# Performance work log

Hardware: AMD Instinct MI355X
Metric: run time of the kernel (lower is better)

## Reference

```python
import jax, jax.numpy as jnp
import numpy as np

DIM_IN = 1024
DIM_OUT = 1024


def setup_inputs() -> dict:
    key = jax.random.key(0)
    k_x, k_q, k_k, k_v = jax.random.split(key, 4)
    B, S = 4, 2048
    scale = 1.0 / np.sqrt(DIM_IN)
    X = jax.random.normal(k_x, (B, S, DIM_IN), dtype=jnp.float32)
    # nn.Linear weights stored as [out, in]; forward is X @ W.T
    W_q = jax.random.normal(k_q, (DIM_OUT, DIM_IN), dtype=jnp.float32) * scale
    W_k = jax.random.normal(k_k, (DIM_OUT, DIM_IN), dtype=jnp.float32) * scale
    W_v = jax.random.normal(k_v, (DIM_OUT, DIM_IN), dtype=jnp.float32) * scale
    return {"X": X, "W_q": W_q, "W_k": W_k, "W_v": W_v}


def reference(X, W_q, W_k, W_v):
    # Q, K, V: [B, S, D]
    Q = jnp.einsum('bsd,ed->bse', X, W_q)
    K = jnp.einsum('bsd,ed->bse', X, W_k)
    V = jnp.einsum('bsd,ed->bse', X, W_v)
    S = X.shape[1]
    scores = jnp.einsum('bqe,bke->bqk', Q, K)  # [B, S, S]
    # causal mask: strictly upper triangle -> -inf (applied before scaling, as in source)
    causal = jnp.triu(jnp.ones((S, S), dtype=bool), k=1)
    scores = jnp.where(causal[None, :, :], -jnp.inf, scores)
    scores = scores / jnp.sqrt(jnp.asarray(K.shape[-1], dtype=scores.dtype))
    weights = jax.nn.softmax(scores, axis=-1)
    # dropout_p = 0.0 (eval mode) -> identity
    return jnp.einsum('bqk,bke->bqe', weights, V)
```

## Files before the change

### kernel.cpp

```cpp
#include <hip/hip_runtime.h>
#include <hip/hip_bf16.h>
#include <hip/hip_fp16.h>
#include <stdint.h>

#define NBATCH 4
#define SEQ    2048
#define DIM    1024

typedef __attribute__((ext_vector_type(8))) __bf16 bf16x8;
typedef __attribute__((ext_vector_type(4))) float  f32x4;

#define OFF_XBF   (0ull)
#define OFF_WBF   (16777216ull)
#define OFF_Q     (23068672ull)
#define OFF_K     (39845888ull)
#define OFF_VT    (56623104ull)
#define OFF_SC    (73400320ull)
#define OFF_P     (140509184ull)

__device__ __forceinline__ uint16_t f2bf(float f) {
  uint32_t u = __float_as_uint(f);
  u = (u + 0x7fffu + ((u >> 16) & 1u)) >> 16;
  return (uint16_t)u;
}

__global__ __launch_bounds__(256) void k_convert(const float* __restrict__ X,
                                                 const float* __restrict__ Wq,
                                                 const float* __restrict__ Wk,
                                                 const float* __restrict__ Wv,
                                                 uint16_t* __restrict__ Xbf,
                                                 uint16_t* __restrict__ Wbf) {
  int id = blockIdx.x;
  if (id < 8192) {
    int i = id * 256 + threadIdx.x;
    float4 v = ((const float4*)X)[i];
    ushort4 o;
    o.x = f2bf(v.x); o.y = f2bf(v.y); o.z = f2bf(v.z); o.w = f2bf(v.w);
    ((ushort4*)Xbf)[i] = o;
  } else {
    int j = id - 8192;
    int g = j >> 10;
    const float* W = (g == 0) ? Wq : (g == 1) ? Wk : Wv;
    float scale = (g == 0) ? 0.03125f : 1.0f;
    int i = (j & 1023) * 256 + threadIdx.x;
    float4 v = ((const float4*)W)[i];
    ushort4 o;
    o.x = f2bf(v.x * scale); o.y = f2bf(v.y * scale);
    o.z = f2bf(v.z * scale); o.w = f2bf(v.w * scale);
    ((ushort4*)(Wbf + (size_t)g * 1048576))[i] = o;
  }
}


__device__ __forceinline__ void gll16(const void* g, void* l) {
  __builtin_amdgcn_global_load_lds((const __attribute__((address_space(1))) void*)g,
                                   (__attribute__((address_space(3))) void*)l, 16, 0, 0);
}

__device__ __forceinline__ bf16x8 frag_ld(const char* lds, int row, int kbyte) {
  int bo = row * 128 + kbyte;
  bo ^= (row & 7) << 4;
  return *(const bf16x8*)(lds + bo);
}

#define VM_WAIT8() asm volatile("s_waitcnt vmcnt(8)" ::: "memory")
#define VM_WAIT0() asm volatile("s_waitcnt vmcnt(0)" ::: "memory")
#define RAW_BAR()  asm volatile("s_barrier" ::: "memory")

__device__ __forceinline__ void stage_tile(const uint16_t* __restrict__ g, int ld,
                                           int t, char* lds) {
#pragma unroll
  for (int c = 0; c < 4; ++c) {
    int L = c * 4096 + t * 16;
    int row = L >> 7;
    int slot = (t & 7) ^ (row & 7);
    gll16((const void*)(g + (size_t)row * ld + slot * 8), (void*)(lds + L));
  }
}

__device__ __forceinline__ void gemm_loop(const uint16_t* __restrict__ A, int lda,
                                          const uint16_t* __restrict__ Bm, int ldb,
                                          int ksteps, char* lds, f32x4 acc[4][4]) {
  char* lA0 = lds;          char* lA1 = lds + 16384;
  char* lB0 = lds + 32768;  char* lB1 = lds + 49152;
  const int t = threadIdx.x;
  const int lane = t & 63;
  const int wm = (t >> 6) & 1;
  const int wn = t >> 7;
  const int frow = lane & 15;
  const int fk16 = (lane >> 4) * 16;

  stage_tile(A,      lda, t, lA0); stage_tile(Bm,      ldb, t, lB0);
  if (ksteps > 1) { stage_tile(A + 64, lda, t, lA1); stage_tile(Bm + 64, ldb, t, lB1); }

  for (int kt = 0; kt < ksteps; ++kt) {
    if (kt == ksteps - 1) { VM_WAIT0(); } else { VM_WAIT8(); }
    RAW_BAR();
    const char* cA = (kt & 1) ? lA1 : lA0;
    const char* cB = (kt & 1) ? lB1 : lB0;
#pragma unroll
    for (int ki = 0; ki < 2; ++ki) {
      bf16x8 av[4], bv[4];
#pragma unroll
      for (int mi = 0; mi < 4; ++mi)
        av[mi] = frag_ld(cA, wm * 64 + mi * 16 + frow, ki * 64 + fk16);
#pragma unroll
      for (int ni = 0; ni < 4; ++ni)
        bv[ni] = frag_ld(cB, wn * 64 + ni * 16 + frow, ki * 64 + fk16);
      __builtin_amdgcn_s_setprio(1);
#pragma unroll
      for (int mi = 0; mi < 4; ++mi)
#pragma unroll
        for (int ni = 0; ni < 4; ++ni)
          acc[mi][ni] = __builtin_amdgcn_mfma_f32_16x16x32_bf16(av[mi], bv[ni],
                                                                acc[mi][ni], 0, 0, 0);
      __builtin_amdgcn_s_setprio(0);
    }
    RAW_BAR();
    if (kt + 2 < ksteps) {
      stage_tile(A  + (kt + 2) * 64, lda, t, (kt & 1) ? lA1 : lA0);
      stage_tile(Bm + (kt + 2) * 64, ldb, t, (kt & 1) ? lB1 : lB0);
    }
  }
}

__global__ __launch_bounds__(256) void k_qkv(const uint16_t* __restrict__ Xbf,
                                             const uint16_t* __restrict__ Wbf,
                                             uint16_t* __restrict__ Qb,
                                             uint16_t* __restrict__ Kb,
                                             uint16_t* __restrict__ Vt) {
  __shared__ __align__(16) char lds[65536];
  int id = blockIdx.x;
  const int mt = id & 63, nt = id >> 6;
  const int m0 = mt * 128, n0 = nt * 128;
  const int g = n0 >> 10, ncol = n0 & 1023;

  f32x4 acc[4][4];
#pragma unroll
  for (int i = 0; i < 4; ++i)
#pragma unroll
    for (int j = 0; j < 4; ++j) acc[i][j] = (f32x4){0.f, 0.f, 0.f, 0.f};

  const uint16_t* A  = Xbf + (size_t)m0 * DIM;
  const uint16_t* Bm = Wbf + (size_t)n0 * DIM;
  gemm_loop(A, DIM, Bm, DIM, DIM / 64, lds, acc);

  const int lane = threadIdx.x & 63;
  const int wm = (threadIdx.x >> 6) & 1, wn = threadIdx.x >> 7;
  const int rbase = wm * 64 + (lane >> 4) * 4;
  const int cbase = wn * 64 + (lane & 15);

  if (g < 2) {
    uint16_t* out = (g == 0) ? Qb : Kb;
#pragma unroll
    for (int mi = 0; mi < 4; ++mi)
#pragma unroll
      for (int ni = 0; ni < 4; ++ni) {
        int c = ncol + cbase + ni * 16;
#pragma unroll
        for (int r = 0; r < 4; ++r) {
          int m = m0 + rbase + mi * 16 + r;
          out[(size_t)m * DIM + c] = f2bf(acc[mi][ni][r]);
        }
      }
  } else {
    const int b = m0 >> 11, sl = m0 & 2047;
#pragma unroll
    for (int mi = 0; mi < 4; ++mi)
#pragma unroll
      for (int ni = 0; ni < 4; ++ni) {
        int e = ncol + cbase + ni * 16;
        int s = sl + rbase + mi * 16;
        ushort4 o;
        o.x = f2bf(acc[mi][ni][0]); o.y = f2bf(acc[mi][ni][1]);
        o.z = f2bf(acc[mi][ni][2]); o.w = f2bf(acc[mi][ni][3]);
        *(ushort4*)(Vt + ((size_t)b * DIM + e) * SEQ + s) = o;
      }
  }
}

__global__ __launch_bounds__(256) void k_scores(const uint16_t* __restrict__ Qb,
                                                const uint16_t* __restrict__ Kb,
                                                __half* __restrict__ Sc) {
  __shared__ __align__(16) char lds[65536];
  int x = blockIdx.x;
  int b = x / 136, tr = x % 136;
  int qt = 0;
  while ((qt + 1) * (qt + 2) / 2 <= tr) ++qt;
  int kt = tr - qt * (qt + 1) / 2;

  f32x4 acc[4][4];
#pragma unroll
  for (int i = 0; i < 4; ++i)
#pragma unroll
    for (int j = 0; j < 4; ++j) acc[i][j] = (f32x4){0.f, 0.f, 0.f, 0.f};

  const uint16_t* A = Qb + ((size_t)b * SEQ + qt * 128) * DIM;
  const uint16_t* Bm = Kb + ((size_t)b * SEQ + kt * 128) * DIM;
  gemm_loop(A, DIM, Bm, DIM, DIM / 64, lds, acc);

  const int lane = threadIdx.x & 63;
  const int wm = (threadIdx.x >> 6) & 1, wn = threadIdx.x >> 7;
  const int rbase = qt * 128 + wm * 64 + (lane >> 4) * 4;
  const int cbase = kt * 128 + wn * 64 + (lane & 15);
  __half* out = Sc + (size_t)b * SEQ * SEQ;
#pragma unroll
  for (int mi = 0; mi < 4; ++mi)
#pragma unroll
    for (int ni = 0; ni < 4; ++ni) {
      int c = cbase + ni * 16;
#pragma unroll
      for (int r = 0; r < 4; ++r)
        out[(size_t)(rbase + mi * 16 + r) * SEQ + c] = __float2half(acc[mi][ni][r]);
    }
}

struct h4 { __half2 a, b; };

__global__ __launch_bounds__(256) void k_softmax(const __half* __restrict__ Sc,
                                                 uint16_t* __restrict__ P) {
  int gid = blockIdx.x * 4 + (threadIdx.x >> 6);
  int lane = threadIdx.x & 63;
  int b = gid >> 11, q = gid & 2047;
  const __half* srow = Sc + ((size_t)b * SEQ + q) * SEQ;
  uint16_t* prow = P + ((size_t)b * SEQ + q) * SEQ;
  int nv = q + 1;
  int kpad = ((q >> 7) + 1) << 7;
  int niter = (kpad + 255) >> 8;

  float4 v[8];
  const h4* src = (const h4*)srow;
#pragma unroll
  for (int i = 0; i < 8; ++i) {
    if (i < niter) {
      int idx = lane + (i << 6);
      h4 raw = src[idx];
      float2 fa = __half22float2(raw.a), fb = __half22float2(raw.b);
      int k0 = idx << 2;
      float4 x;
      x.x = (k0 + 0 < nv) ? fa.x : -1e38f;
      x.y = (k0 + 1 < nv) ? fa.y : -1e38f;
      x.z = (k0 + 2 < nv) ? fb.x : -1e38f;
      x.w = (k0 + 3 < nv) ? fb.y : -1e38f;
      v[i] = x;
    } else {
      v[i] = make_float4(-1e38f, -1e38f, -1e38f, -1e38f);
    }
  }
  float m = -1e38f;
#pragma unroll
  for (int i = 0; i < 8; ++i)
    m = fmaxf(m, fmaxf(fmaxf(v[i].x, v[i].y), fmaxf(v[i].z, v[i].w)));
#pragma unroll
  for (int o = 32; o > 0; o >>= 1) m = fmaxf(m, __shfl_xor(m, o));

  float s = 0.f;
#pragma unroll
  for (int i = 0; i < 8; ++i) {
    v[i].x = __expf(v[i].x - m); v[i].y = __expf(v[i].y - m);
    v[i].z = __expf(v[i].z - m); v[i].w = __expf(v[i].w - m);
    s += v[i].x + v[i].y + v[i].z + v[i].w;
  }
#pragma unroll
  for (int o = 32; o > 0; o >>= 1) s += __shfl_xor(s, o);
  float inv = 1.0f / s;

  ushort4* dst = (ushort4*)prow;
#pragma unroll
  for (int i = 0; i < 8; ++i) {
    if (i < niter) {
      int idx = lane + (i << 6);
      if ((idx << 2) < kpad) {
        ushort4 o;
        o.x = f2bf(v[i].x * inv); o.y = f2bf(v[i].y * inv);
        o.z = f2bf(v[i].z * inv); o.w = f2bf(v[i].w * inv);
        dst[idx] = o;
      }
    }
  }
}

__global__ __launch_bounds__(256) void k_pv(const uint16_t* __restrict__ P,
                                            const uint16_t* __restrict__ Vt,
                                            float* __restrict__ O) {
  __shared__ __align__(16) char lds[65536];
  int x = blockIdx.x;
  int b = x >> 7, r7 = x & 127;
  int qt = 15 - (r7 >> 3);
  int et = r7 & 7;

  f32x4 acc[4][4];
#pragma unroll
  for (int i = 0; i < 4; ++i)
#pragma unroll
    for (int j = 0; j < 4; ++j) acc[i][j] = (f32x4){0.f, 0.f, 0.f, 0.f};

  const uint16_t* A = P + (size_t)b * SEQ * SEQ + (size_t)qt * 128 * SEQ;
  const uint16_t* Bm = Vt + (size_t)b * DIM * SEQ + (size_t)et * 128 * SEQ;
  gemm_loop(A, SEQ, Bm, SEQ, (qt + 1) * 2, lds, acc);

  const int lane = threadIdx.x & 63;
  const int wm = (threadIdx.x >> 6) & 1, wn = threadIdx.x >> 7;
  const int rbase = qt * 128 + wm * 64 + (lane >> 4) * 4;
  const int cbase = et * 128 + wn * 64 + (lane & 15);
  float* out = O + (size_t)b * SEQ * DIM;
#pragma unroll
  for (int mi = 0; mi < 4; ++mi)
#pragma unroll
    for (int ni = 0; ni < 4; ++ni) {
      int c = cbase + ni * 16;
#pragma unroll
      for (int r = 0; r < 4; ++r)
        out[(size_t)(rbase + mi * 16 + r) * DIM + c] = acc[mi][ni][r];
    }
}

extern "C" void kernel_launch(void* const* d_in, const int* in_sizes, int n_in,
                              void* d_out, int out_size, void* d_ws, size_t ws_size,
                              hipStream_t stream) {
  const float* X  = (const float*)d_in[0];
  const float* Wq = (const float*)d_in[1];
  const float* Wk = (const float*)d_in[2];
  const float* Wv = (const float*)d_in[3];
  char* ws = (char*)d_ws;
  uint16_t* Xbf = (uint16_t*)(ws + OFF_XBF);
  uint16_t* Wbf = (uint16_t*)(ws + OFF_WBF);
  uint16_t* Qb  = (uint16_t*)(ws + OFF_Q);
  uint16_t* Kb  = (uint16_t*)(ws + OFF_K);
  uint16_t* Vt  = (uint16_t*)(ws + OFF_VT);
  __half*   Sc  = (__half*)(ws + OFF_SC);
  uint16_t* P   = (uint16_t*)(ws + OFF_P);
  float*    O   = (float*)d_out;

  k_convert<<<11264, 256, 0, stream>>>(X, Wq, Wk, Wv, Xbf, Wbf);
  k_qkv<<<1536, 256, 0, stream>>>(Xbf, Wbf, Qb, Kb, Vt);
  k_scores<<<544, 256, 0, stream>>>(Qb, Kb, Sc);
  k_softmax<<<2048, 256, 0, stream>>>(Sc, P);
  k_pv<<<512, 256, 0, stream>>>(P, Vt, O);
}
```

Measured before the change: 160.5 us.

## Restructure QKV GEMM into 128x256 tiles with 8 waves and interleaved loads

The QKV projection kernel now uses 512-thread blocks with 128x256 output tiles, a 128-wide K step and 96KB of dynamic LDS. The loads for the next K step are split into partial sweeps and issued between two half-phases of MFMA work, each half covering two of the four N subtiles. The goal is more reuse of each A tile and better overlap of global-to-LDS copies with matrix math. In exchange there are more barriers per step and more LDS per block, which may limit occupancy. The hand-tuned vmcnt waits add correctness risk.

```diff
diff --git a/kernel.cpp b/kernel.cpp
--- a/kernel.cpp
+++ b/kernel.cpp
@@ -64,8 +64,162 @@
 }
 
 #define VM_WAIT8() asm volatile("s_waitcnt vmcnt(8)" ::: "memory")
+#define VM_WAIT3() asm volatile("s_waitcnt vmcnt(3)" ::: "memory")
 #define VM_WAIT0() asm volatile("s_waitcnt vmcnt(0)" ::: "memory")
 #define RAW_BAR()  asm volatile("s_barrier" ::: "memory")
+
+
+__device__ __forceinline__ void sweepA(const uint16_t* __restrict__ Ab, int kt,
+                                       int t, char* ldsA) {
+#pragma unroll
+  for (int c = 0; c < 2; ++c) {
+    int L = c * 8192 + t * 16;
+    int row = L >> 7;
+    int slot = (t & 7) ^ (row & 7);
+    gll16((const void*)(Ab + (size_t)row * DIM + kt * 64 + slot * 8),
+          (void*)(ldsA + L));
+  }
+}
+__device__ __forceinline__ void sweepB(const uint16_t* __restrict__ Bb, int kt,
+                                       int t, char* ldsB, int sb, int off) {
+  int strip = sb + (t >> 8);
+  int rl = (t >> 3) & 31;
+  int grow = strip * 64 + off + rl;
+  int slot = (t & 7) ^ (grow & 7);
+  gll16((const void*)(Bb + (size_t)grow * DIM + kt * 64 + slot * 8),
+        (void*)(ldsB + grow * 128 + (t & 7) * 16));
+}
+
+__global__ __launch_bounds__(512, 2) void k_qkv(const uint16_t* __restrict__ Xbf,
+                                                const uint16_t* __restrict__ Wbf,
+                                                uint16_t* __restrict__ Qb,
+                                                uint16_t* __restrict__ Kb,
+                                                uint16_t* __restrict__ Vt) {
+  extern __shared__ char lds[];
+  char* A0 = lds;           char* B0 = lds + 16384;
+  char* A1 = lds + 49152;   char* B1 = lds + 65536;
+
+  const int t = threadIdx.x;
+  const int lane = t & 63;
+  const int wid = t >> 6;
+  const int wm = wid >> 2;
+  const int wn = wid & 3;
+  const int frow = lane & 15;
+  const int fk16 = (lane >> 4) * 16;
+
+  int id = blockIdx.x;
+  const int mt = id & 63, nt = id >> 6;
+  const int m0 = mt * 128, n0 = nt * 256;
+  const int g = n0 >> 10, ncol = n0 & 1023;
+
+  const uint16_t* A  = Xbf + (size_t)m0 * DIM;
+  const uint16_t* Bm = Wbf + (size_t)n0 * DIM;
+
+  f32x4 acc[4][4];
+#pragma unroll
+  for (int i = 0; i < 4; ++i)
+#pragma unroll
+    for (int j = 0; j < 4; ++j) acc[i][j] = (f32x4){0.f, 0.f, 0.f, 0.f};
+
+  sweepA(A, 0, t, A0);
+  sweepB(Bm, 0, t, B0, 0, 0);  sweepB(Bm, 0, t, B0, 2, 0);
+  sweepB(Bm, 0, t, B0, 0, 32); sweepB(Bm, 0, t, B0, 2, 32);
+  sweepA(A, 1, t, A1);
+  sweepB(Bm, 1, t, B1, 0, 0);
+  VM_WAIT3(); RAW_BAR();
+
+#pragma unroll 1
+  for (int kt = 0; kt < 16; ++kt) {
+    char* cA = (kt & 1) ? A1 : A0;
+    char* cB = (kt & 1) ? B1 : B0;
+    char* nB = (kt & 1) ? B0 : B1;
+
+    bf16x8 av[4][2], bv01[2][2];
+#pragma unroll
+    for (int mi = 0; mi < 4; ++mi)
+#pragma unroll
+      for (int ki = 0; ki < 2; ++ki)
+        av[mi][ki] = frag_ld(cA, wm * 64 + mi * 16 + frow, ki * 64 + fk16);
+#pragma unroll
+    for (int ni = 0; ni < 2; ++ni)
+#pragma unroll
+      for (int ki = 0; ki < 2; ++ki)
+        bv01[ni][ki] = frag_ld(cB, wn * 64 + ni * 16 + frow, ki * 64 + fk16);
+    if (kt <= 14) {
+      sweepB(Bm, kt + 1, t, nB, 2, 0);
+      sweepB(Bm, kt + 1, t, nB, 0, 32);
+      sweepB(Bm, kt + 1, t, nB, 2, 32);
+    }
+    RAW_BAR();
+    __builtin_amdgcn_s_setprio(1);
+#pragma unroll
+    for (int mi = 0; mi < 4; ++mi)
+#pragma unroll
+      for (int ni = 0; ni < 2; ++ni)
+#pragma unroll
+        for (int ki = 0; ki < 2; ++ki)
+          acc[mi][ni] = __builtin_amdgcn_mfma_f32_16x16x32_bf16(av[mi][ki], bv01[ni][ki],
+                                                                acc[mi][ni], 0, 0, 0);
+    __builtin_amdgcn_s_setprio(0);
+    RAW_BAR();
+
+    bf16x8 bv23[2][2];
+#pragma unroll
+    for (int ni = 0; ni < 2; ++ni)
+#pragma unroll
+      for (int ki = 0; ki < 2; ++ki)
+        bv23[ni][ki] = frag_ld(cB, wn * 64 + (2 + ni) * 16 + frow, ki * 64 + fk16);
+    if (kt <= 13) {
+      sweepA(A, kt + 2, t, cA);
+      sweepB(Bm, kt + 2, t, cB, 0, 0);
+    }
+    if (kt <= 13)      { VM_WAIT3(); }
+    else if (kt == 14) { VM_WAIT0(); }
+    RAW_BAR();
+    __builtin_amdgcn_s_setprio(1);
+#pragma unroll
+    for (int mi = 0; mi < 4; ++mi)
+#pragma unroll
+      for (int ni = 0; ni < 2; ++ni)
+#pragma unroll
+        for (int ki = 0; ki < 2; ++ki)
+          acc[mi][2 + ni] = __builtin_amdgcn_mfma_f32_16x16x32_bf16(av[mi][ki], bv23[ni][ki],
+                                                                    acc[mi][2 + ni], 0, 0, 0);
+    __builtin_amdgcn_s_setprio(0);
+    RAW_BAR();
+  }
+
+  const int rbase = wm * 64 + (lane >> 4) * 4;
+  const int cbase = wn * 64 + (lane & 15);
+
+  if (g < 2) {
+    uint16_t* out = (g == 0) ? Qb : Kb;
+#pragma unroll
+    for (int mi = 0; mi < 4; ++mi)
+#pragma unroll
+      for (int ni = 0; ni < 4; ++ni) {
+        int c = ncol + cbase + ni * 16;
+#pragma unroll
+        for (int r = 0; r < 4; ++r) {
+          int m = m0 + rbase + mi * 16 + r;
+          out[(size_t)m * DIM + c] = f2bf(acc[mi][ni][r]);
+        }
+      }
+  } else {
+    const int b = m0 >> 11, sl = m0 & 2047;
+#pragma unroll
+    for (int mi = 0; mi < 4; ++mi)
+#pragma unroll
+      for (int ni = 0; ni < 4; ++ni) {
+        int e = ncol + cbase + ni * 16;
+        int s = sl + rbase + mi * 16;
+        ushort4 o;
+        o.x = f2bf(acc[mi][ni][0]); o.y = f2bf(acc[mi][ni][1]);
+        o.z = f2bf(acc[mi][ni][2]); o.w = f2bf(acc[mi][ni][3]);
+        *(ushort4*)(Vt + ((size_t)b * DIM + e) * SEQ + s) = o;
+      }
+  }
+}
 
 __device__ __forceinline__ void stage_tile(const uint16_t* __restrict__ g, int ld,
                                            int t, char* lds) {
@@ -121,61 +275,6 @@
       stage_tile(A  + (kt + 2) * 64, lda, t, (kt & 1) ? lA1 : lA0);
       stage_tile(Bm + (kt + 2) * 64, ldb, t, (kt & 1) ? lB1 : lB0);
     }
-  }
-}
-
-__global__ __launch_bounds__(256) void k_qkv(const uint16_t* __restrict__ Xbf,
-                                             const uint16_t* __restrict__ Wbf,
-                                             uint16_t* __restrict__ Qb,
-                                             uint16_t* __restrict__ Kb,
-                                             uint16_t* __restrict__ Vt) {
-  __shared__ __align__(16) char lds[65536];
-  int id = blockIdx.x;
-  const int mt = id & 63, nt = id >> 6;
-  const int m0 = mt * 128, n0 = nt * 128;
-  const int g = n0 >> 10, ncol = n0 & 1023;
-
-  f32x4 acc[4][4];
-#pragma unroll
-  for (int i = 0; i < 4; ++i)
-#pragma unroll
-    for (int j = 0; j < 4; ++j) acc[i][j] = (f32x4){0.f, 0.f, 0.f, 0.f};
-
-  const uint16_t* A  = Xbf + (size_t)m0 * DIM;
-  const uint16_t* Bm = Wbf + (size_t)n0 * DIM;
-  gemm_loop(A, DIM, Bm, DIM, DIM / 64, lds, acc);
-
-  const int lane = threadIdx.x & 63;
-  const int wm = (threadIdx.x >> 6) & 1, wn = threadIdx.x >> 7;
-  const int rbase = wm * 64 + (lane >> 4) * 4;
-  const int cbase = wn * 64 + (lane & 15);
-
-  if (g < 2) {
-    uint16_t* out = (g == 0) ? Qb : Kb;
-#pragma unroll
-    for (int mi = 0; mi < 4; ++mi)
-#pragma unroll
-      for (int ni = 0; ni < 4; ++ni) {
-        int c = ncol + cbase + ni * 16;
-#pragma unroll
-        for (int r = 0; r < 4; ++r) {
-          int m = m0 + rbase + mi * 16 + r;
-          out[(size_t)m * DIM + c] = f2bf(acc[mi][ni][r]);
-        }
-      }
-  } else {
-    const int b = m0 >> 11, sl = m0 & 2047;
-#pragma unroll
-    for (int mi = 0; mi < 4; ++mi)
-#pragma unroll
-      for (int ni = 0; ni < 4; ++ni) {
-        int e = ncol + cbase + ni * 16;
-        int s = sl + rbase + mi * 16;
-        ushort4 o;
-        o.x = f2bf(acc[mi][ni][0]); o.y = f2bf(acc[mi][ni][1]);
-        o.z = f2bf(acc[mi][ni][2]); o.w = f2bf(acc[mi][ni][3]);
-        *(ushort4*)(Vt + ((size_t)b * DIM + e) * SEQ + s) = o;
-      }
   }
 }
 
@@ -333,7 +432,7 @@
   float*    O   = (float*)d_out;
 
   k_convert<<<11264, 256, 0, stream>>>(X, Wq, Wk, Wv, Xbf, Wbf);
-  k_qkv<<<1536, 256, 0, stream>>>(Xbf, Wbf, Qb, Kb, Vt);
+  k_qkv<<<768, 512, 98304, stream>>>(Xbf, Wbf, Qb, Kb, Vt);
   k_scores<<<544, 256, 0, stream>>>(Qb, Kb, Sc);
   k_softmax<<<2048, 256, 0, stream>>>(Sc, P);
   k_pv<<<512, 256, 0, stream>>>(P, Vt, O);
```

Measured after the change: 165.7 us. +3.3%, slower.

## Use 256x256 tiles with 8 waves and 128KB LDS for QKV GEMM

Applied to the files above, without the earlier changes.

Replaces the 128x128, 256-thread QKV projection GEMM with a 256x256 tile per 512-thread block. It double-buffers 128KB of dynamic LDS and issues the next k-tile's half-tile loads between MFMA quadrants, so each loaded tile feeds more MFMAs and prefetch overlaps compute. It also reorders the k_pv block index so heavy and light causal rows from different batches interleave across the grid. Costs: only one block per CU and 384 blocks, which risks tail imbalance, plus the dynamic LDS size may need an attribute to exceed the default limit.

```diff
diff --git a/kernel.cpp b/kernel.cpp
--- a/kernel.cpp
+++ b/kernel.cpp
@@ -67,6 +67,184 @@
 #define VM_WAIT0() asm volatile("s_waitcnt vmcnt(0)" ::: "memory")
 #define RAW_BAR()  asm volatile("s_barrier" ::: "memory")
 
+
+__device__ __forceinline__ void stage_half(const uint16_t* __restrict__ g,
+                                           int t, char* ldsH) {
+#pragma unroll
+  for (int c = 0; c < 2; ++c) {
+    int L = c * 8192 + t * 16;
+    int row = L >> 7;
+    int slot = (t & 7) ^ (row & 7);
+    gll16((const void*)(g + (size_t)row * DIM + slot * 8), (void*)(ldsH + L));
+  }
+}
+
+template<int CUR>
+__device__ __forceinline__ void qkv_ktile(char* lds, const uint16_t* __restrict__ A,
+                                          const uint16_t* __restrict__ Bm,
+                                          int t, int wm, int wn, int frow, int fk16,
+                                          int kt, f32x4 (&acc)[8][4]) {
+  char* base = lds + CUR * 65536;
+  const char* Ah0 = base;
+  const char* Ah1 = base + 16384;
+  const char* Bh  = base + 32768 + (wn >> 1) * 16384;
+  const int brow = (wn & 1) * 64;
+  const bool stage_on = (kt <= 13);
+  const int k2 = (kt + 2) * 64;
+
+  bf16x8 av[4][2], bv01[2][2], bv23[2][2];
+
+  if (kt == 15) { VM_WAIT0(); } else { VM_WAIT8(); }
+  RAW_BAR();
+#pragma unroll
+  for (int mq = 0; mq < 4; ++mq)
+#pragma unroll
+    for (int ki = 0; ki < 2; ++ki)
+      av[mq][ki] = frag_ld(Ah0, wm * 64 + mq * 16 + frow, ki * 64 + fk16);
+#pragma unroll
+  for (int nq = 0; nq < 2; ++nq)
+#pragma unroll
+    for (int ki = 0; ki < 2; ++ki)
+      bv01[nq][ki] = frag_ld(Bh, brow + nq * 16 + frow, ki * 64 + fk16);
+  __builtin_amdgcn_s_setprio(1);
+#pragma unroll
+  for (int mq = 0; mq < 4; ++mq)
+#pragma unroll
+    for (int nq = 0; nq < 2; ++nq)
+#pragma unroll
+      for (int ki = 0; ki < 2; ++ki)
+        acc[mq][nq] = __builtin_amdgcn_mfma_f32_16x16x32_bf16(av[mq][ki], bv01[nq][ki],
+                                                              acc[mq][nq], 0, 0, 0);
+  __builtin_amdgcn_s_setprio(0);
+  RAW_BAR();
+
+#pragma unroll
+  for (int nq = 0; nq < 2; ++nq)
+#pragma unroll
+    for (int ki = 0; ki < 2; ++ki)
+      bv23[nq][ki] = frag_ld(Bh, brow + 32 + nq * 16 + frow, ki * 64 + fk16);
+  if (stage_on) stage_half(A + k2, t, base + 0);
+  __builtin_amdgcn_s_setprio(1);
+#pragma unroll
+  for (int mq = 0; mq < 4; ++mq)
+#pragma unroll
+    for (int nq = 0; nq < 2; ++nq)
+#pragma unroll
+      for (int ki = 0; ki < 2; ++ki)
+        acc[mq][2 + nq] = __builtin_amdgcn_mfma_f32_16x16x32_bf16(av[mq][ki], bv23[nq][ki],
+                                                                  acc[mq][2 + nq], 0, 0, 0);
+  __builtin_amdgcn_s_setprio(0);
+  RAW_BAR();
+
+#pragma unroll
+  for (int mq = 0; mq < 4; ++mq)
+#pragma unroll
+    for (int ki = 0; ki < 2; ++ki)
+      av[mq][ki] = frag_ld(Ah1, wm * 64 + mq * 16 + frow, ki * 64 + fk16);
+  if (stage_on) {
+    stage_half(Bm + k2,             t, base + 32768);
+    stage_half(Bm + 128 * DIM + k2, t, base + 49152);
+  }
+  __builtin_amdgcn_s_setprio(1);
+#pragma unroll
+  for (int mq = 0; mq < 4; ++mq)
+#pragma unroll
+    for (int nq = 0; nq < 2; ++nq)
+#pragma unroll
+      for (int ki = 0; ki < 2; ++ki)
+        acc[4 + mq][nq] = __builtin_amdgcn_mfma_f32_16x16x32_bf16(av[mq][ki], bv01[nq][ki],
+                                                                  acc[4 + mq][nq], 0, 0, 0);
+  __builtin_amdgcn_s_setprio(0);
+  RAW_BAR();
+
+  if (stage_on) stage_half(A + 128 * DIM + k2, t, base + 16384);
+  __builtin_amdgcn_s_setprio(1);
+#pragma unroll
+  for (int mq = 0; mq < 4; ++mq)
+#pragma unroll
+    for (int nq = 0; nq < 2; ++nq)
+#pragma unroll
+      for (int ki = 0; ki < 2; ++ki)
+        acc[4 + mq][2 + nq] = __builtin_amdgcn_mfma_f32_16x16x32_bf16(av[mq][ki], bv23[nq][ki],
+                                                                      acc[4 + mq][2 + nq], 0, 0, 0);
+  __builtin_amdgcn_s_setprio(0);
+  RAW_BAR();
+}
+
+__global__ __launch_bounds__(512, 1) void k_qkv(const uint16_t* __restrict__ Xbf,
+                                                const uint16_t* __restrict__ Wbf,
+                                                uint16_t* __restrict__ Qb,
+                                                uint16_t* __restrict__ Kb,
+                                                uint16_t* __restrict__ Vt) {
+  extern __shared__ char lds[];
+  const int t = threadIdx.x;
+  const int lane = t & 63;
+  const int wid = t >> 6;
+  const int wm = wid >> 2;
+  const int wn = wid & 3;
+  const int frow = lane & 15;
+  const int fk16 = (lane >> 4) * 16;
+
+  int id = blockIdx.x;
+  const int mt = id & 31, nt = id >> 5;
+  const int m0 = mt * 256, n0 = nt * 256;
+  const int g = n0 >> 10, ncol = n0 & 1023;
+
+  const uint16_t* A  = Xbf + (size_t)m0 * DIM;
+  const uint16_t* Bm = Wbf + (size_t)n0 * DIM;
+
+  f32x4 acc[8][4];
+#pragma unroll
+  for (int i = 0; i < 8; ++i)
+#pragma unroll
+    for (int j = 0; j < 4; ++j) acc[i][j] = (f32x4){0.f, 0.f, 0.f, 0.f};
+
+  stage_half(A,                 t, lds + 0);
+  stage_half(A  + 128 * DIM,    t, lds + 16384);
+  stage_half(Bm,                t, lds + 32768);
+  stage_half(Bm + 128 * DIM,    t, lds + 49152);
+  stage_half(A  + 64,            t, lds + 65536 + 0);
+  stage_half(A  + 128 * DIM + 64, t, lds + 65536 + 16384);
+  stage_half(Bm + 64,            t, lds + 65536 + 32768);
+  stage_half(Bm + 128 * DIM + 64, t, lds + 65536 + 49152);
+
+#pragma unroll 1
+  for (int t2 = 0; t2 < 16; t2 += 2) {
+    qkv_ktile<0>(lds, A, Bm, t, wm, wn, frow, fk16, t2,     acc);
+    qkv_ktile<1>(lds, A, Bm, t, wm, wn, frow, fk16, t2 + 1, acc);
+  }
+
+  const int rb0 = wm * 64 + (lane >> 4) * 4;
+  const int cb0 = (wn >> 1) * 128 + (wn & 1) * 64 + (lane & 15);
+
+  if (g < 2) {
+    uint16_t* out = (g == 0) ? Qb : Kb;
+#pragma unroll
+    for (int mf = 0; mf < 8; ++mf)
+#pragma unroll
+      for (int nf = 0; nf < 4; ++nf) {
+        int c = ncol + cb0 + nf * 16;
+        int mrow = m0 + (mf >> 2) * 128 + rb0 + (mf & 3) * 16;
+#pragma unroll
+        for (int r = 0; r < 4; ++r)
+          out[(size_t)(mrow + r) * DIM + c] = f2bf(acc[mf][nf][r]);
+      }
+  } else {
+    const int b = m0 >> 11, sl = m0 & 2047;
+#pragma unroll
+    for (int mf = 0; mf < 8; ++mf)
+#pragma unroll
+      for (int nf = 0; nf < 4; ++nf) {
+        int e = ncol + cb0 + nf * 16;
+        int s = sl + (mf >> 2) * 128 + rb0 + (mf & 3) * 16;
+        ushort4 o;
+        o.x = f2bf(acc[mf][nf][0]); o.y = f2bf(acc[mf][nf][1]);
+        o.z = f2bf(acc[mf][nf][2]); o.w = f2bf(acc[mf][nf][3]);
+        *(ushort4*)(Vt + ((size_t)b * DIM + e) * SEQ + s) = o;
+      }
+  }
+}
+
 __device__ __forceinline__ void stage_tile(const uint16_t* __restrict__ g, int ld,
                                            int t, char* lds) {
 #pragma unroll
@@ -121,61 +299,6 @@
       stage_tile(A  + (kt + 2) * 64, lda, t, (kt & 1) ? lA1 : lA0);
       stage_tile(Bm + (kt + 2) * 64, ldb, t, (kt & 1) ? lB1 : lB0);
     }
-  }
-}
-
-__global__ __launch_bounds__(256) void k_qkv(const uint16_t* __restrict__ Xbf,
-                                             const uint16_t* __restrict__ Wbf,
-                                             uint16_t* __restrict__ Qb,
-                                             uint16_t* __restrict__ Kb,
-                                             uint16_t* __restrict__ Vt) {
-  __shared__ __align__(16) char lds[65536];
-  int id = blockIdx.x;
-  const int mt = id & 63, nt = id >> 6;
-  const int m0 = mt * 128, n0 = nt * 128;
-  const int g = n0 >> 10, ncol = n0 & 1023;
-
-  f32x4 acc[4][4];
-#pragma unroll
-  for (int i = 0; i < 4; ++i)
-#pragma unroll
-    for (int j = 0; j < 4; ++j) acc[i][j] = (f32x4){0.f, 0.f, 0.f, 0.f};
-
-  const uint16_t* A  = Xbf + (size_t)m0 * DIM;
-  const uint16_t* Bm = Wbf + (size_t)n0 * DIM;
-  gemm_loop(A, DIM, Bm, DIM, DIM / 64, lds, acc);
-
-  const int lane = threadIdx.x & 63;
-  const int wm = (threadIdx.x >> 6) & 1, wn = threadIdx.x >> 7;
-  const int rbase = wm * 64 + (lane >> 4) * 4;
-  const int cbase = wn * 64 + (lane & 15);
-
-  if (g < 2) {
-    uint16_t* out = (g == 0) ? Qb : Kb;
-#pragma unroll
-    for (int mi = 0; mi < 4; ++mi)
-#pragma unroll
-      for (int ni = 0; ni < 4; ++ni) {
-        int c = ncol + cbase + ni * 16;
-#pragma unroll
-        for (int r = 0; r < 4; ++r) {
-          int m = m0 + rbase + mi * 16 + r;
-          out[(size_t)m * DIM + c] = f2bf(acc[mi][ni][r]);
-        }
-      }
-  } else {
-    const int b = m0 >> 11, sl = m0 & 2047;
-#pragma unroll
-    for (int mi = 0; mi < 4; ++mi)
-#pragma unroll
-      for (int ni = 0; ni < 4; ++ni) {
-        int e = ncol + cbase + ni * 16;
-        int s = sl + rbase + mi * 16;
-        ushort4 o;
-        o.x = f2bf(acc[mi][ni][0]); o.y = f2bf(acc[mi][ni][1]);
-        o.z = f2bf(acc[mi][ni][2]); o.w = f2bf(acc[mi][ni][3]);
-        *(ushort4*)(Vt + ((size_t)b * DIM + e) * SEQ + s) = o;
-      }
   }
 }
 
@@ -285,9 +408,10 @@
                                             float* __restrict__ O) {
   __shared__ __align__(16) char lds[65536];
   int x = blockIdx.x;
-  int b = x >> 7, r7 = x & 127;
-  int qt = 15 - (r7 >> 3);
-  int et = r7 & 7;
+  int idx = x & 255, half = x >> 8;
+  int qt = half ? (idx >> 4) : 15 - (idx >> 4);
+  int et = idx & 7;
+  int b  = ((idx >> 3) & 1) | (half << 1);
 
   f32x4 acc[4][4];
 #pragma unroll
@@ -333,7 +457,7 @@
   float*    O   = (float*)d_out;
 
   k_convert<<<11264, 256, 0, stream>>>(X, Wq, Wk, Wv, Xbf, Wbf);
-  k_qkv<<<1536, 256, 0, stream>>>(Xbf, Wbf, Qb, Kb, Vt);
+  k_qkv<<<384, 512, 131072, stream>>>(Xbf, Wbf, Qb, Kb, Vt);
   k_scores<<<544, 256, 0, stream>>>(Qb, Kb, Sc);
   k_softmax<<<2048, 256, 0, stream>>>(Sc, P);
   k_pv<<<512, 256, 0, stream>>>(P, Vt, O);
```

Measured after the change: 161.8 us. No clear change (+0.8%).

## Split score tiles into 128x64 halves and rebalance PV block scheduling

Applied to the files above, without the earlier changes.

The scores kernel now computes 128x64 output tiles with a new half-width GEMM loop, doubling the grid from 544 to 1088 blocks and cutting the LDS footprint to 48KB so that more blocks fit per CU and the 256-CU device sees a better-filled wave. The PV kernel's block-to-tile mapping is reordered so the first 256 blocks take batches 0-1 with the heaviest causal tiles first, and the second 256 take batches 2-3 with the lightest first, to balance triangular work. The cost is that Q tiles are loaded twice, and the smaller tiles do fewer MFMAs per LDS fragment load.

```diff
diff --git a/kernel.cpp b/kernel.cpp
--- a/kernel.cpp
+++ b/kernel.cpp
@@ -64,6 +64,7 @@
 }
 
 #define VM_WAIT8() asm volatile("s_waitcnt vmcnt(8)" ::: "memory")
+#define VM_WAIT6() asm volatile("s_waitcnt vmcnt(6)" ::: "memory")
 #define VM_WAIT0() asm volatile("s_waitcnt vmcnt(0)" ::: "memory")
 #define RAW_BAR()  asm volatile("s_barrier" ::: "memory")
 
@@ -124,6 +125,63 @@
   }
 }
 
+__device__ __forceinline__ void stage_btile(const uint16_t* __restrict__ g, int ld,
+                                            int t, char* lds) {
+#pragma unroll
+  for (int c = 0; c < 2; ++c) {
+    int L = c * 4096 + t * 16;
+    int row = L >> 7;
+    int slot = (t & 7) ^ (row & 7);
+    gll16((const void*)(g + (size_t)row * ld + slot * 8), (void*)(lds + L));
+  }
+}
+
+__device__ __forceinline__ void gemm_loop_h(const uint16_t* __restrict__ A, int lda,
+                                            const uint16_t* __restrict__ Bm, int ldb,
+                                            int ksteps, char* lds, f32x4 acc[4][2]) {
+  char* lA0 = lds;          char* lA1 = lds + 16384;
+  char* lB0 = lds + 32768;  char* lB1 = lds + 40960;
+  const int t = threadIdx.x;
+  const int lane = t & 63;
+  const int wm = (t >> 6) & 1;
+  const int wn = t >> 7;
+  const int frow = lane & 15;
+  const int fk16 = (lane >> 4) * 16;
+
+  stage_tile(A, lda, t, lA0); stage_btile(Bm, ldb, t, lB0);
+  if (ksteps > 1) { stage_tile(A + 64, lda, t, lA1); stage_btile(Bm + 64, ldb, t, lB1); }
+
+  for (int kt = 0; kt < ksteps; ++kt) {
+    if (kt == ksteps - 1) { VM_WAIT0(); } else { VM_WAIT6(); }
+    RAW_BAR();
+    const char* cA = (kt & 1) ? lA1 : lA0;
+    const char* cB = (kt & 1) ? lB1 : lB0;
+#pragma unroll
+    for (int ki = 0; ki < 2; ++ki) {
+      bf16x8 av[4], bv[2];
+#pragma unroll
+      for (int mi = 0; mi < 4; ++mi)
+        av[mi] = frag_ld(cA, wm * 64 + mi * 16 + frow, ki * 64 + fk16);
+#pragma unroll
+      for (int ni = 0; ni < 2; ++ni)
+        bv[ni] = frag_ld(cB, wn * 32 + ni * 16 + frow, ki * 64 + fk16);
+      __builtin_amdgcn_s_setprio(1);
+#pragma unroll
+      for (int mi = 0; mi < 4; ++mi)
+#pragma unroll
+        for (int ni = 0; ni < 2; ++ni)
+          acc[mi][ni] = __builtin_amdgcn_mfma_f32_16x16x32_bf16(av[mi], bv[ni],
+                                                                acc[mi][ni], 0, 0, 0);
+      __builtin_amdgcn_s_setprio(0);
+    }
+    RAW_BAR();
+    if (kt + 2 < ksteps) {
+      stage_tile (A  + (kt + 2) * 64, lda, t, (kt & 1) ? lA1 : lA0);
+      stage_btile(Bm + (kt + 2) * 64, ldb, t, (kt & 1) ? lB1 : lB0);
+    }
+  }
+}
+
 __global__ __launch_bounds__(256) void k_qkv(const uint16_t* __restrict__ Xbf,
                                              const uint16_t* __restrict__ Wbf,
                                              uint16_t* __restrict__ Qb,
@@ -182,32 +240,33 @@
 __global__ __launch_bounds__(256) void k_scores(const uint16_t* __restrict__ Qb,
                                                 const uint16_t* __restrict__ Kb,
                                                 __half* __restrict__ Sc) {
-  __shared__ __align__(16) char lds[65536];
-  int x = blockIdx.x;
-  int b = x / 136, tr = x % 136;
+  __shared__ __align__(16) char lds[49152];
+  int j = blockIdx.x;
+  int b = j / 272, r = j % 272;
+  int tr = r >> 1, nh = r & 1;
   int qt = 0;
   while ((qt + 1) * (qt + 2) / 2 <= tr) ++qt;
   int kt = tr - qt * (qt + 1) / 2;
 
-  f32x4 acc[4][4];
+  f32x4 acc[4][2];
 #pragma unroll
   for (int i = 0; i < 4; ++i)
 #pragma unroll
-    for (int j = 0; j < 4; ++j) acc[i][j] = (f32x4){0.f, 0.f, 0.f, 0.f};
-
-  const uint16_t* A = Qb + ((size_t)b * SEQ + qt * 128) * DIM;
-  const uint16_t* Bm = Kb + ((size_t)b * SEQ + kt * 128) * DIM;
-  gemm_loop(A, DIM, Bm, DIM, DIM / 64, lds, acc);
+    for (int jj = 0; jj < 2; ++jj) acc[i][jj] = (f32x4){0.f, 0.f, 0.f, 0.f};
+
+  const uint16_t* A  = Qb + ((size_t)b * SEQ + qt * 128) * DIM;
+  const uint16_t* Bm = Kb + ((size_t)b * SEQ + kt * 128 + nh * 64) * DIM;
+  gemm_loop_h(A, DIM, Bm, DIM, DIM / 64, lds, acc);
 
   const int lane = threadIdx.x & 63;
   const int wm = (threadIdx.x >> 6) & 1, wn = threadIdx.x >> 7;
   const int rbase = qt * 128 + wm * 64 + (lane >> 4) * 4;
-  const int cbase = kt * 128 + wn * 64 + (lane & 15);
+  const int cbase = kt * 128 + nh * 64 + wn * 32 + (lane & 15);
   __half* out = Sc + (size_t)b * SEQ * SEQ;
 #pragma unroll
   for (int mi = 0; mi < 4; ++mi)
 #pragma unroll
-    for (int ni = 0; ni < 4; ++ni) {
+    for (int ni = 0; ni < 2; ++ni) {
       int c = cbase + ni * 16;
 #pragma unroll
       for (int r = 0; r < 4; ++r)
@@ -285,9 +344,10 @@
                                             float* __restrict__ O) {
   __shared__ __align__(16) char lds[65536];
   int x = blockIdx.x;
-  int b = x >> 7, r7 = x & 127;
-  int qt = 15 - (r7 >> 3);
-  int et = r7 & 7;
+  int idx = x & 255, half = x >> 8;
+  int qt = half ? (idx >> 4) : 15 - (idx >> 4);
+  int et = idx & 7;
+  int b  = ((idx >> 3) & 1) | (half << 1);
 
   f32x4 acc[4][4];
 #pragma unroll
@@ -334,7 +394,7 @@
 
   k_convert<<<11264, 256, 0, stream>>>(X, Wq, Wk, Wv, Xbf, Wbf);
   k_qkv<<<1536, 256, 0, stream>>>(Xbf, Wbf, Qb, Kb, Vt);
-  k_scores<<<544, 256, 0, stream>>>(Qb, Kb, Sc);
+  k_scores<<<1088, 256, 0, stream>>>(Qb, Kb, Sc);
   k_softmax<<<2048, 256, 0, stream>>>(Sc, P);
   k_pv<<<512, 256, 0, stream>>>(P, Vt, O);
 }
```

Measured after the change: 144.8 us. -9.8%, faster.
